# Kernel optimization log

Hardware: AMD Instinct MI355X
Metric: run time of the kernel (lower is better)

The kernel has to match this reference:

```python
import jax, jax.numpy as jnp
import numpy as np

B, T, H, V = 64, 48, 512, 32000


def _uni(k, shape, fan_in):
    s = 1.0 / np.sqrt(fan_in)
    return jax.random.uniform(k, shape, jnp.float32, -s, s)


def setup_inputs() -> dict:
    key = jax.random.key(0)
    ks = jax.random.split(key, 21)
    inp = {
        "feat": jax.random.normal(ks[0], (B, T, H), jnp.float32),
        "caption": jax.random.normal(ks[1], (B, T, H), jnp.float32),
        "ids": jax.random.randint(ks[2], (B, T), 0, V),
    }
    i = 3
    for name, in_dim in (("1", H), ("2", 2 * H), ("d1", H), ("d2", 2 * H)):
        inp["w_ih" + name] = _uni(ks[i], (4 * H, in_dim), H); i += 1
        inp["w_hh" + name] = _uni(ks[i], (4 * H, H), H); i += 1
        inp["b_ih" + name] = _uni(ks[i], (4 * H,), H); i += 1
        inp["b_hh" + name] = _uni(ks[i], (4 * H,), H); i += 1
    inp["w_o"] = _uni(ks[i], (V, H), H); i += 1
    inp["b_o"] = _uni(ks[i], (V,), H)
    return inp


def lstm_cell(x, h, c, w_ih, w_hh, b_ih, b_hh):
    # PyTorch LSTMCell: gates in i, f, g, o order
    g = x @ w_ih.T + b_ih + h @ w_hh.T + b_hh
    gi, gf, gg, go = jnp.split(g, 4, axis=-1)
    c_new = jax.nn.sigmoid(gf) * c + jax.nn.sigmoid(gi) * jnp.tanh(gg)
    h_new = jax.nn.sigmoid(go) * jnp.tanh(c_new)
    return h_new, c_new


def reference(feat, caption, ids,
              w_ih1, w_hh1, b_ih1, b_hh1,
              w_ih2, w_hh2, b_ih2, b_hh2,
              w_ihd1, w_hhd1, b_ihd1, b_hhd1,
              w_ihd2, w_hhd2, b_ihd2, b_hhd2,
              w_o, b_o):
    pad = jnp.zeros((B, H), feat.dtype)
    z = jnp.zeros((B, H), feat.dtype)

    def enc_step(carry, x):
        h1, c1, h2, c2 = carry
        h1, c1 = lstm_cell(x, h1, c1, w_ih1, w_hh1, b_ih1, b_hh1)
        h2, c2 = lstm_cell(jnp.concatenate([pad, h1], 1), h2, c2,
                           w_ih2, w_hh2, b_ih2, b_hh2)
        return (h1, c1, h2, c2), None

    carry, _ = jax.lax.scan(enc_step, (z, z, z, z), jnp.swapaxes(feat, 0, 1))

    def dec_step(carry, xs):
        h1, c1, h2, c2 = carry
        cap, tgt = xs
        h1, c1 = lstm_cell(pad, h1, c1, w_ihd1, w_hhd1, b_ihd1, b_hhd1)
        h2, c2 = lstm_cell(jnp.concatenate([cap, h1], 1), h2, c2,
                           w_ihd2, w_hhd2, b_ihd2, b_hhd2)
        logits = h2 @ w_o.T + b_o  # [B, V]
        lp = jax.nn.log_softmax(logits, axis=-1)
        ce = -jnp.take_along_axis(lp, tgt[:, None], axis=1)[:, 0].mean()
        return (h1, c1, h2, c2), ce

    caps = jnp.swapaxes(caption[:, : T - 1, :], 0, 1)  # [T-1, B, H]
    tgts = jnp.swapaxes(ids[:, 1:T], 0, 1)             # [T-1, B]
    _, ces = jax.lax.scan(dec_step, carry, (caps, tgts))
    # total_loss += sum(mean_ce) / batch_size (word_loss is already a mean)
    return jnp.sum(ces) / B
```

## Files before the change

kernel.cpp:

```cpp
#include <hip/hip_runtime.h>
#include <math.h>

#define B_ 64
#define T_ 48
#define H_ 512
#define V_ 32000
#define G_ 2048
#define BH_ (B_*H_)
#define BG_ (B_*G_)

typedef short short8 __attribute__((ext_vector_type(8)));
typedef float f32x4 __attribute__((ext_vector_type(4)));

__device__ __forceinline__ float sigmoidf_(float x){ return 1.f/(1.f+__expf(-x)); }

__device__ __forceinline__ unsigned short f2bf(float f){
  unsigned u = __float_as_uint(f);
  u += 0x7fffu + ((u>>16)&1u);
  return (unsigned short)(u>>16);
}
__device__ __forceinline__ float bf2f(unsigned short u){
  return __uint_as_float(((unsigned)u)<<16);
}

__device__ __forceinline__ short8 cvt8(const float* g){
  float4 a = *(const float4*)g;
  float4 b = *(const float4*)(g+4);
  short8 v;
  v[0]=(short)f2bf(a.x); v[1]=(short)f2bf(a.y); v[2]=(short)f2bf(a.z); v[3]=(short)f2bf(a.w);
  v[4]=(short)f2bf(b.x); v[5]=(short)f2bf(b.y); v[6]=(short)f2bf(b.z); v[7]=(short)f2bf(b.w);
  return v;
}

__global__ void init_kernel(unsigned short* h1_0, unsigned short* h2_0, unsigned* flags){
  int i = blockIdx.x*256 + threadIdx.x;
  short8 z = {0,0,0,0,0,0,0,0};
  if (i < 4096) ((short8*)h1_0)[i] = z;
  else          ((short8*)h2_0)[i-4096] = z;
  if (i < 1152) flags[i] = 0u;
}

__global__ void cvt_cat_kernel(const float* __restrict__ s0, int ld0, int off0,
                               const float* __restrict__ s1, int ld1, int off1,
                               unsigned short* __restrict__ dst, int dld, long total8)
{
  int cols8 = dld >> 3;
  for (long i = blockIdx.x*256 + threadIdx.x; i < total8; i += (long)gridDim.x*256){
    int r = (int)(i / cols8);
    int k = (int)(i - (long)r*cols8) * 8;
    short8 v = (k < 512 || !s1) ? cvt8(s0 + (long)r*ld0 + off0 + k)
                                : cvt8(s1 + (long)r*ld1 + off1 + (k-512));
    *(short8*)(dst + (long)r*dld + k) = v;
  }
}

__global__ void bias_sum_kernel(const float* a1, const float* a2, float* o1,
                                const float* b1, const float* b2, float* o2){
  int n = blockIdx.x*256 + threadIdx.x;
  if (n < G_){ o1[n] = a1[n] + a2[n]; o2[n] = b1[n] + b2[n]; }
}

__global__ __launch_bounds__(512,1) void mm_pre_kernel(
    const float* __restrict__ A, int a_bstride,
    const unsigned short* __restrict__ Wbf,
    const float* __restrict__ bA, const float* __restrict__ bB,
    unsigned short* __restrict__ out)
{
  const int s = blockIdx.x, n0 = blockIdx.y*256;
  const int t = threadIdx.x, w = t>>6, l = t&63, ln = l&15, lk = l>>4;
  __shared__ short8 smA[64*64];
  __shared__ short8 smB[256*8];

  const float* af32 = A + (long)s*H_;

  f32x4 acc[4][2];
#pragma unroll
  for (int mf=0; mf<4; ++mf)
#pragma unroll
    for (int nf=0; nf<2; ++nf) acc[mf][nf] = (f32x4){0.f,0.f,0.f,0.f};

#pragma unroll
  for (int i=0;i<8;++i){ int e=i*4096+t*8; int m=e>>9, k=e&511;
    smA[m*64 + ((k>>3)^(m&7))] = cvt8(&af32[(long)m*a_bstride + k]); }

  for (int kc=0; kc<8; ++kc){
    __syncthreads();
#pragma unroll
    for (int i=0;i<4;++i){ int e=i*4096+t*8; int n=e>>6, k=e&63;
      smB[n*8 + ((k>>3)^(n&7))] = *(const short8*)(Wbf + (long)(n0+n)*512 + kc*64 + k); }
    __syncthreads();
#pragma unroll
    for (int ks2=0; ks2<2; ++ks2){
#pragma unroll
      for (int nf=0; nf<2; ++nf){
        int n = w*32 + nf*16 + ln;
        short8 bfr = smB[n*8 + ((ks2*4+lk)^(n&7))];
#pragma unroll
        for (int mf=0; mf<4; ++mf){
          int m = mf*16+ln;
          short8 afr = smA[m*64 + (((kc*2+ks2)*4+lk)^(m&7))];
          acc[mf][nf] = __builtin_amdgcn_mfma_f32_16x16x32_bf16(afr, bfr, acc[mf][nf], 0,0,0);
        }
      }
    }
  }
#pragma unroll
  for (int nf=0; nf<2; ++nf){
    int n = n0 + w*32 + nf*16 + ln;
    float bias = bA[n] + bB[n];
#pragma unroll
    for (int mf=0; mf<4; ++mf)
#pragma unroll
      for (int r=0; r<4; ++r){
        int m = mf*16 + lk*4 + r;
        out[(long)s*BG_ + (long)m*G_ + n] = f2bf(acc[mf][nf][r] + bias);
      }
  }
}

__global__ __launch_bounds__(256,1) void fused_chain_kernel(
    const unsigned short* __restrict__ w1e, const unsigned short* __restrict__ w1d,
    const unsigned short* __restrict__ w2e, const unsigned short* __restrict__ w2d,
    const unsigned short* __restrict__ x1b,
    const unsigned short* __restrict__ capqb,
    const float* __restrict__ bd1s, const float* __restrict__ b2es,
    unsigned short* __restrict__ h1, unsigned short* __restrict__ h2,
    unsigned* __restrict__ flags)
{
  const int bc = blockIdx.x;
  const int isL2 = (bc >= 32);
  const int cb = bc & 31;
  const int t = threadIdx.x;
  const int wv = t>>6, l = t&63, ln = l&15, lk = l>>4;

  __shared__ short8 smA[64*128];
  __shared__ float gbuf[4][16][68];
  __shared__ float c_lds[16][68];
  unsigned short* stash = (unsigned short*)&smA[0];

  short8 W[32];
  const int col = wv*512 + cb*16 + ln;
  if (isL2){
    const long wrow = (long)col * 1024;
#pragma unroll
    for (int ks=0; ks<32; ++ks) W[ks] = *(const short8*)(w2e + wrow + ks*32 + lk*8);
  } else {
    const long wrow = (long)col * 512;
#pragma unroll
    for (int ks=0; ks<16; ++ks){
      W[ks]    = *(const short8*)(w1e + wrow + ks*32 + lk*8);
      W[16+ks] = *(const short8*)(w1d + wrow + ks*32 + lk*8);
    }
  }
  const float bext = isL2 ? b2es[col] : bd1s[col];

  for (int i=t; i<16*68; i+=256) (&c_lds[0][0])[i] = 0.f;

  for (int s=0; s<96; ++s){
    if (isL2 && s == 49){
      const long wrow = (long)col * 1024;
#pragma unroll
      for (int ks=0; ks<32; ++ks) W[ks] = *(const short8*)(w2d + wrow + ks*32 + lk*8);
    }
    const int active = isL2 ? (s>=1) : (s<95);
    if (active){
      if (!isL2){
        const unsigned short* hp = h1 + (long)s*BH_;
#pragma unroll
        for (int i=0;i<16;++i){ int e=i*2048+t*8; int m=e>>9, k=e&511;
          smA[m*128 + ((k>>3)^(m&7))] = *(const short8*)(hp + m*512 + k); }
      } else {
        const unsigned short* hpA = h2 + (long)(s-1)*BH_;
        const unsigned short* hpB = h1 + (long)s*BH_;
#pragma unroll
        for (int i=0;i<16;++i){ int e=i*2048+t*8; int m=e>>9, k=e&511;
          smA[m*128 + ((k>>3)^(m&7))]      = *(const short8*)(hpA + m*512 + k);
          smA[m*128 + ((k>>3)^(m&7)) + 64] = *(const short8*)(hpB + m*512 + k);
        }
      }

      const int dec = isL2 ? ((s-1)>=48) : (s>=48);
      float prev[4][4];
      if (!isL2){
        if (s < 48){
          const unsigned short* pp = x1b + (long)s*BG_ + col;
#pragma unroll
          for (int mf=0;mf<4;++mf)
#pragma unroll
            for (int r=0;r<4;++r) prev[mf][r] = bf2f(pp[(long)(mf*16+lk*4+r)*G_]);
        } else {
#pragma unroll
          for (int mf=0;mf<4;++mf)
#pragma unroll
            for (int r=0;r<4;++r) prev[mf][r] = bext;
        }
      } else {
        int s2 = s-1;
        if (s2 < 48){
#pragma unroll
          for (int mf=0;mf<4;++mf)
#pragma unroll
            for (int r=0;r<4;++r) prev[mf][r] = bext;
        } else {
          const unsigned short* pp = capqb + (long)(s2-48)*BG_ + col;
#pragma unroll
          for (int mf=0;mf<4;++mf)
#pragma unroll
            for (int r=0;r<4;++r) prev[mf][r] = bf2f(pp[(long)(mf*16+lk*4+r)*G_]);
        }
      }
      __syncthreads();

      f32x4 acc[4];
#pragma unroll
      for (int mf=0;mf<4;++mf) acc[mf] = (f32x4){0.f,0.f,0.f,0.f};

      if (isL2){
#pragma unroll
        for (int ks=0; ks<32; ++ks)
#pragma unroll
          for (int mf=0; mf<4; ++mf){
            int m = mf*16+ln;
            acc[mf] = __builtin_amdgcn_mfma_f32_16x16x32_bf16(
              smA[m*128 + ((ks*4+lk)^(m&7))], W[ks], acc[mf], 0,0,0);
          }
      } else if (!dec){
#pragma unroll
        for (int ks=0; ks<16; ++ks)
#pragma unroll
          for (int mf=0; mf<4; ++mf){
            int m = mf*16+ln;
            acc[mf] = __builtin_amdgcn_mfma_f32_16x16x32_bf16(
              smA[m*128 + ((ks*4+lk)^(m&7))], W[ks], acc[mf], 0,0,0);
          }
      } else {
#pragma unroll
        for (int ks=0; ks<16; ++ks)
#pragma unroll
          for (int mf=0; mf<4; ++mf){
            int m = mf*16+ln;
            acc[mf] = __builtin_amdgcn_mfma_f32_16x16x32_bf16(
              smA[m*128 + ((ks*4+lk)^(m&7))], W[16+ks], acc[mf], 0,0,0);
          }
      }

#pragma unroll
      for (int mf=0;mf<4;++mf)
#pragma unroll
        for (int r=0;r<4;++r) acc[mf][r] += prev[mf][r];

#pragma unroll
      for (int mf=0;mf<4;++mf) *(f32x4*)&gbuf[wv][ln][mf*16+lk*4] = acc[mf];
      __syncthreads();

      {
        int n = t&15, m0 = (t>>4)*4;
        float4 gi = *(float4*)&gbuf[0][n][m0];
        float4 gf = *(float4*)&gbuf[1][n][m0];
        float4 gg = *(float4*)&gbuf[2][n][m0];
        float4 go = *(float4*)&gbuf[3][n][m0];
        float4 c4 = *(float4*)&c_lds[n][m0];
        float cn[4];
        float a_i[4]={gi.x,gi.y,gi.z,gi.w}, a_f[4]={gf.x,gf.y,gf.z,gf.w};
        float a_g[4]={gg.x,gg.y,gg.z,gg.w}, a_o[4]={go.x,go.y,go.z,go.w};
        float ci[4]={c4.x,c4.y,c4.z,c4.w};
#pragma unroll
        for (int j=0;j<4;++j){
          float i_ = sigmoidf_(a_i[j]), f_ = sigmoidf_(a_f[j]), o_ = sigmoidf_(a_o[j]);
          float g_ = tanhf(a_g[j]);
          cn[j] = f_*ci[j] + i_*g_;
          stash[(m0+j)*24 + n] = f2bf(o_*tanhf(cn[j]));
        }
        *(float4*)&c_lds[n][m0] = make_float4(cn[0],cn[1],cn[2],cn[3]);
      }
      __syncthreads();
      {
        unsigned short* ho = (isL2 ? (h2 + (long)s*BH_) : (h1 + (long)(s+1)*BH_)) + cb*16;
        int m = t>>2, q = t&3;
        unsigned long long v = *(const unsigned long long*)&stash[m*24 + q*4];
        __hip_atomic_store((unsigned long long*)(ho + (long)m*512 + q*4), v,
                           __ATOMIC_RELAXED, __HIP_MEMORY_SCOPE_AGENT);
      }
    }

    if (s < 95){
      unsigned g = (unsigned)(s+1);
      __syncthreads();
      if (t == 0)
        __hip_atomic_store(&flags[bc*16], g, __ATOMIC_RELAXED, __HIP_MEMORY_SCOPE_AGENT);
      if (t < 64){
        while (__hip_atomic_load(&flags[t*16], __ATOMIC_RELAXED, __HIP_MEMORY_SCOPE_AGENT) < g)
          __builtin_amdgcn_s_sleep(1);
      }
      __syncthreads();
    }
  }
}

__global__ __launch_bounds__(512,1) void ce_vt_kernel(
    const unsigned short* __restrict__ h2_bf, const unsigned short* __restrict__ wo_bf,
    const float* __restrict__ b_o, const int* __restrict__ ids,
    float* __restrict__ partial, float* __restrict__ tgt)
{
  const int vt = blockIdx.x, v0 = vt*128;
  const int t = threadIdx.x, wv = t>>6, l = t&63, ln = l&15, lk = l>>4;
  __shared__ short8 smB[128*64];
  __shared__ short8 smAc[64*8];
  __shared__ float red[8][64];
  __shared__ int tid_s[64];

  for (int i = t; i < 128*64; i += 512){
    int n = i >> 6, c = i & 63;
    smB[n*64 + ((c & 56) | ((c & 7) ^ (n & 7)))] =
        *(const short8*)(wo_bf + (long)(v0+n)*512 + c*8);
  }
  const int nn = wv*16 + ln;
  const float bo = b_o[v0 + nn];
  __syncthreads();

  for (int td = 0; td < 47; ++td){
    if (t < 64) tid_s[t] = ids[t*T_ + td + 1];
    const unsigned short* hp = h2_bf + (long)(49+td)*BH_;

    f32x4 acc[4];
#pragma unroll
    for (int mf=0;mf<4;++mf) acc[mf] = (f32x4){0.f,0.f,0.f,0.f};

    for (int kc=0; kc<8; ++kc){
      __syncthreads();
      { int m = t>>3, c = t&7;
        smAc[m*8 + (c ^ (m&7))] = *(const short8*)(hp + m*512 + kc*64 + c*8); }
      __syncthreads();
#pragma unroll
      for (int ks2=0; ks2<2; ++ks2){
        short8 bfr = smB[nn*64 + kc*8 + ((ks2*4+lk)^(nn&7))];
#pragma unroll
        for (int mf=0; mf<4; ++mf){
          int m = mf*16+ln;
          short8 afr = smAc[m*8 + ((ks2*4+lk)^(m&7))];
          acc[mf] = __builtin_amdgcn_mfma_f32_16x16x32_bf16(afr, bfr, acc[mf], 0,0,0);
        }
      }
    }

    float se[4][4];
#pragma unroll
    for (int mf=0; mf<4; ++mf)
#pragma unroll
      for (int r=0;r<4;++r){
        int m = mf*16 + lk*4 + r;
        float lg = acc[mf][r] + bo;
        se[mf][r] = __expf(lg);
        if (v0 + nn == tid_s[m]) tgt[td*64 + m] = lg;
      }
#pragma unroll
    for (int off=1; off<16; off<<=1)
#pragma unroll
      for (int mf=0; mf<4; ++mf)
#pragma unroll
        for (int r=0;r<4;++r) se[mf][r] += __shfl_xor(se[mf][r], off);
    if (ln == 0){
#pragma unroll
      for (int mf=0; mf<4; ++mf)
        *(f32x4*)&red[wv][mf*16 + lk*4] = (f32x4){se[mf][0],se[mf][1],se[mf][2],se[mf][3]};
    }
    __syncthreads();
    if (t < 64){
      float ssum = 0.f;
#pragma unroll
      for (int w2=0; w2<8; ++w2) ssum += red[w2][t];
      partial[(long)vt*3008 + td*64 + t] = ssum;
    }
  }
}

__global__ void ce_combine(const float* __restrict__ partial, const float* __restrict__ tgt,
                           float* __restrict__ ce_row){
  int r = blockIdx.x*256 + threadIdx.x;
  if (r < 3008){
    float s = 0.f;
    for (int i=0;i<250;++i) s += partial[(long)i*3008 + r];
    ce_row[r] = __logf(s) - tgt[r];
  }
}

__global__ void ce_final(const float* __restrict__ ce_row, float* __restrict__ out){
  __shared__ float red[256];
  float s = 0.f;
  for (int i=threadIdx.x; i<3008; i+=256) s += ce_row[i];
  red[threadIdx.x] = s;
  __syncthreads();
  for (int off=128; off>0; off>>=1){
    if (threadIdx.x < off) red[threadIdx.x] += red[threadIdx.x + off];
    __syncthreads();
  }
  if (threadIdx.x == 0) out[0] = red[0] * (1.0f/4096.0f);
}

extern "C" void kernel_launch(void* const* d_in, const int* in_sizes, int n_in,
                              void* d_out, int out_size, void* d_ws, size_t ws_size,
                              hipStream_t stream)
{
  (void)in_sizes; (void)n_in; (void)out_size; (void)ws_size;
  const float* feat    = (const float*)d_in[0];
  const float* caption = (const float*)d_in[1];
  const int*   ids     = (const int*)d_in[2];
  const float* w_ih1  = (const float*)d_in[3];
  const float* w_hh1  = (const float*)d_in[4];
  const float* b_ih1  = (const float*)d_in[5];
  const float* b_hh1  = (const float*)d_in[6];
  const float* w_ih2  = (const float*)d_in[7];
  const float* w_hh2  = (const float*)d_in[8];
  const float* b_ih2  = (const float*)d_in[9];
  const float* b_hh2  = (const float*)d_in[10];
  const float* w_hhd1 = (const float*)d_in[12];
  const float* b_ihd1 = (const float*)d_in[13];
  const float* b_hhd1 = (const float*)d_in[14];
  const float* w_ihd2 = (const float*)d_in[15];
  const float* w_hhd2 = (const float*)d_in[16];
  const float* b_ihd2 = (const float*)d_in[17];
  const float* b_hhd2 = (const float*)d_in[18];
  const float* w_o    = (const float*)d_in[19];
  const float* b_o    = (const float*)d_in[20];

  char* p = (char*)d_ws;
  unsigned short* h1    = (unsigned short*)p; p += 96L*BH_*2;
  unsigned short* h2    = (unsigned short*)p; p += 96L*BH_*2;
  unsigned short* w2e   = (unsigned short*)p; p += 2048L*1024*2;
  unsigned short* w2d   = (unsigned short*)p; p += 2048L*1024*2;
  char* alias0 = p;
  unsigned short* w1e   = (unsigned short*)p; p += 2048L*512*2;
  unsigned short* w1d   = (unsigned short*)p; p += 2048L*512*2;
  unsigned short* wx1   = (unsigned short*)p; p += 2048L*512*2;
  unsigned short* wcap  = (unsigned short*)p; p += 2048L*512*2;
  unsigned short* x1b   = (unsigned short*)p; p += 48L*BG_*2;
  unsigned short* capqb = (unsigned short*)p; p += 47L*BG_*2;
  unsigned short* wo_bf = (unsigned short*)alias0;
  float* bd1s  = (float*)p; p += 2048*4;
  float* b2es  = (float*)p; p += 2048*4;
  float* partial = (float*)p; p += 250L*3008*4;
  float* tgt   = (float*)p; p += 3008*4;
  float* ce_row= (float*)p; p += 3008*4;
  unsigned* flags = (unsigned*)p; p += 1152*4;

  init_kernel<<<32, 256, 0, stream>>>(h1, h2, flags);

  cvt_cat_kernel<<<256, 256, 0, stream>>>(w_hh1, 512, 0, nullptr, 0, 0, w1e, 512, 2048L*64);
  cvt_cat_kernel<<<256, 256, 0, stream>>>(w_hhd1, 512, 0, nullptr, 0, 0, w1d, 512, 2048L*64);
  cvt_cat_kernel<<<256, 256, 0, stream>>>(w_hh2, 512, 0, w_ih2, 1024, 512, w2e, 1024, 2048L*128);
  cvt_cat_kernel<<<256, 256, 0, stream>>>(w_hhd2, 512, 0, w_ihd2, 1024, 512, w2d, 1024, 2048L*128);
  cvt_cat_kernel<<<256, 256, 0, stream>>>(w_ih1, 512, 0, nullptr, 0, 0, wx1, 512, 2048L*64);
  cvt_cat_kernel<<<256, 256, 0, stream>>>(w_ihd2, 1024, 0, nullptr, 0, 0, wcap, 512, 2048L*64);
  bias_sum_kernel<<<8, 256, 0, stream>>>(b_ihd1, b_hhd1, bd1s, b_ih2, b_hh2, b2es);

  mm_pre_kernel<<<dim3(48,8), 512, 0, stream>>>(feat, T_*H_, wx1, b_ih1, b_hh1, x1b);
  mm_pre_kernel<<<dim3(47,8), 512, 0, stream>>>(caption, T_*H_, wcap, b_ihd2, b_hhd2, capqb);

  fused_chain_kernel<<<64, 256, 0, stream>>>(w1e, w1d, w2e, w2d, x1b, capqb, bd1s, b2es, h1, h2, flags);

  cvt_cat_kernel<<<512, 256, 0, stream>>>(w_o, 512, 0, nullptr, 0, 0, wo_bf, 512, 32000L*64);

  ce_vt_kernel<<<250, 512, 0, stream>>>(h2, wo_bf, b_o, ids, partial, tgt);
  ce_combine<<<12, 256, 0, stream>>>(partial, tgt, ce_row);
  ce_final<<<1, 256, 0, stream>>>(ce_row, (float*)d_out);
}
```

Before: 1.580 ms.

## Overlap decoder CE projection with LSTM chain in persistent mega-kernel

Merges the many weight-conversion, bias and init launches into one prep kernel and combines the two input-projection GEMMs into a single launch. The main change folds the vocabulary-projection cross-entropy into the recurrent chain kernel. 186 extra CE blocks each hold a 128-column slice of w_o in LDS and spin on per-step flags, so they consume each decoder h2 as soon as it is produced instead of waiting for the whole chain. wo_bf no longer aliases the chain weights, which costs extra workspace. The design relies on all 250 blocks being co-resident, or the spinning CE blocks could starve the chain.

```diff
diff --git a/kernel.cpp b/kernel.cpp
--- a/kernel.cpp
+++ b/kernel.cpp
@@ -8,6 +8,7 @@
 #define G_ 2048
 #define BH_ (B_*H_)
 #define BG_ (B_*G_)
+#define NCE_ 186
 
 typedef short short8 __attribute__((ext_vector_type(8)));
 typedef float f32x4 __attribute__((ext_vector_type(4)));
@@ -32,46 +33,71 @@
   return v;
 }
 
-__global__ void init_kernel(unsigned short* h1_0, unsigned short* h2_0, unsigned* flags){
-  int i = blockIdx.x*256 + threadIdx.x;
-  short8 z = {0,0,0,0,0,0,0,0};
-  if (i < 4096) ((short8*)h1_0)[i] = z;
-  else          ((short8*)h2_0)[i-4096] = z;
-  if (i < 1152) flags[i] = 0u;
-}
-
-__global__ void cvt_cat_kernel(const float* __restrict__ s0, int ld0, int off0,
-                               const float* __restrict__ s1, int ld1, int off1,
-                               unsigned short* __restrict__ dst, int dld, long total8)
+#define CEGO_(i) ((64+(i))*16)
+
+__global__ void prep_kernel(
+    const float* __restrict__ w_hh1, const float* __restrict__ w_hhd1,
+    const float* __restrict__ w_hh2, const float* __restrict__ w_ih2,
+    const float* __restrict__ w_hhd2, const float* __restrict__ w_ihd2,
+    const float* __restrict__ w_ih1, const float* __restrict__ w_o,
+    const float* __restrict__ b_ihd1, const float* __restrict__ b_hhd1,
+    const float* __restrict__ b_ih2,  const float* __restrict__ b_hh2,
+    unsigned short* w1e, unsigned short* w1d, unsigned short* w2e, unsigned short* w2d,
+    unsigned short* wx1, unsigned short* wcap, unsigned short* wo_bf,
+    float* bd1s, float* b2es,
+    unsigned short* h1_0, unsigned short* h2_0, unsigned* flags)
 {
-  int cols8 = dld >> 3;
-  for (long i = blockIdx.x*256 + threadIdx.x; i < total8; i += (long)gridDim.x*256){
-    int r = (int)(i / cols8);
-    int k = (int)(i - (long)r*cols8) * 8;
-    short8 v = (k < 512 || !s1) ? cvt8(s0 + (long)r*ld0 + off0 + k)
-                                : cvt8(s1 + (long)r*ld1 + off1 + (k-512));
-    *(short8*)(dst + (long)r*dld + k) = v;
+  const int b = blockIdx.x, t = threadIdx.x;
+  if (b < 64){
+    for (long i = b*256+t; i < 2048L*64; i += 64L*256){ int r=(int)(i>>6), k=(int)(i&63)*8;
+      *(short8*)(w1e + (long)r*512 + k) = cvt8(w_hh1 + (long)r*512 + k); }
+  } else if (b < 128){
+    for (long i = (b-64)*256+t; i < 2048L*64; i += 64L*256){ int r=(int)(i>>6), k=(int)(i&63)*8;
+      *(short8*)(w1d + (long)r*512 + k) = cvt8(w_hhd1 + (long)r*512 + k); }
+  } else if (b < 256){
+    for (long i = (b-128)*256+t; i < 2048L*128; i += 128L*256){ int r=(int)(i>>7), k=(int)(i&127)*8;
+      short8 v = (k<512)? cvt8(w_hh2+(long)r*512+k) : cvt8(w_ih2+(long)r*1024+512+(k-512));
+      *(short8*)(w2e + (long)r*1024 + k) = v; }
+  } else if (b < 384){
+    for (long i = (b-256)*256+t; i < 2048L*128; i += 128L*256){ int r=(int)(i>>7), k=(int)(i&127)*8;
+      short8 v = (k<512)? cvt8(w_hhd2+(long)r*512+k) : cvt8(w_ihd2+(long)r*1024+512+(k-512));
+      *(short8*)(w2d + (long)r*1024 + k) = v; }
+  } else if (b < 448){
+    for (long i = (b-384)*256+t; i < 2048L*64; i += 64L*256){ int r=(int)(i>>6), k=(int)(i&63)*8;
+      *(short8*)(wx1 + (long)r*512 + k) = cvt8(w_ih1 + (long)r*512 + k); }
+  } else if (b < 512){
+    for (long i = (b-448)*256+t; i < 2048L*64; i += 64L*256){ int r=(int)(i>>6), k=(int)(i&63)*8;
+      *(short8*)(wcap + (long)r*512 + k) = cvt8(w_ihd2 + (long)r*1024 + k); }
+  } else if (b < 1012){
+    for (long i = (long)(b-512)*256+t; i < 32000L*64; i += 500L*256){ int r=(int)(i>>6), k=(int)(i&63)*8;
+      *(short8*)(wo_bf + (long)r*512 + k) = cvt8(w_o + (long)r*512 + k); }
+  } else if (b < 1020){
+    int n = (b-1012)*256 + t;
+    bd1s[n] = b_ihd1[n] + b_hhd1[n];
+    b2es[n] = b_ih2[n] + b_hh2[n];
+  } else {
+    short8 z = {0,0,0,0,0,0,0,0};
+    for (int i=(b-1020)*256+t; i<4096; i+=4*256){ ((short8*)h1_0)[i]=z; ((short8*)h2_0)[i]=z; }
+    for (int i=(b-1020)*256+t; i<4096; i+=4*256) flags[i] = 0u;
   }
 }
 
-__global__ void bias_sum_kernel(const float* a1, const float* a2, float* o1,
-                                const float* b1, const float* b2, float* o2){
-  int n = blockIdx.x*256 + threadIdx.x;
-  if (n < G_){ o1[n] = a1[n] + a2[n]; o2[n] = b1[n] + b2[n]; }
-}
-
-__global__ __launch_bounds__(512,1) void mm_pre_kernel(
-    const float* __restrict__ A, int a_bstride,
-    const unsigned short* __restrict__ Wbf,
-    const float* __restrict__ bA, const float* __restrict__ bB,
-    unsigned short* __restrict__ out)
+__global__ __launch_bounds__(512,1) void mm_pre2_kernel(
+    const float* __restrict__ feat, const float* __restrict__ caption,
+    const unsigned short* __restrict__ wx1, const unsigned short* __restrict__ wcap,
+    const float* __restrict__ b_ih1, const float* __restrict__ b_hh1,
+    const float* __restrict__ b_ihd2, const float* __restrict__ b_hhd2,
+    unsigned short* __restrict__ x1b, unsigned short* __restrict__ capqb)
 {
   const int s = blockIdx.x, n0 = blockIdx.y*256;
   const int t = threadIdx.x, w = t>>6, l = t&63, ln = l&15, lk = l>>4;
   __shared__ short8 smA[64*64];
   __shared__ short8 smB[256*8];
 
-  const float* af32 = A + (long)s*H_;
+  const float* af32; const unsigned short* Wbf; const float* bA; const float* bB;
+  unsigned short* out;
+  if (s < 48){ af32 = feat + (long)s*H_;          Wbf = wx1;  bA = b_ih1;  bB = b_hh1;  out = x1b  + (long)s*BG_; }
+  else       { af32 = caption + (long)(s-48)*H_;  Wbf = wcap; bA = b_ihd2; bB = b_hhd2; out = capqb + (long)(s-48)*BG_; }
 
   f32x4 acc[4][2];
 #pragma unroll
@@ -81,7 +107,7 @@
 
 #pragma unroll
   for (int i=0;i<8;++i){ int e=i*4096+t*8; int m=e>>9, k=e&511;
-    smA[m*64 + ((k>>3)^(m&7))] = cvt8(&af32[(long)m*a_bstride + k]); }
+    smA[m*64 + ((k>>3)^(m&7))] = cvt8(&af32[(long)m*(T_*H_) + k]); }
 
   for (int kc=0; kc<8; ++kc){
     __syncthreads();
@@ -113,263 +139,295 @@
 #pragma unroll
       for (int r=0; r<4; ++r){
         int m = mf*16 + lk*4 + r;
-        out[(long)s*BG_ + (long)m*G_ + n] = f2bf(acc[mf][nf][r] + bias);
+        out[(long)m*G_ + n] = f2bf(acc[mf][nf][r] + bias);
       }
   }
 }
 
-__global__ __launch_bounds__(256,1) void fused_chain_kernel(
+__global__ __launch_bounds__(256,1) void mega_kernel(
     const unsigned short* __restrict__ w1e, const unsigned short* __restrict__ w1d,
     const unsigned short* __restrict__ w2e, const unsigned short* __restrict__ w2d,
-    const unsigned short* __restrict__ x1b,
-    const unsigned short* __restrict__ capqb,
+    const unsigned short* __restrict__ x1b, const unsigned short* __restrict__ capqb,
     const float* __restrict__ bd1s, const float* __restrict__ b2es,
     unsigned short* __restrict__ h1, unsigned short* __restrict__ h2,
+    const unsigned short* __restrict__ wo_bf, const float* __restrict__ b_o,
+    const int* __restrict__ ids,
+    float* __restrict__ partial, float* __restrict__ tgt,
     unsigned* __restrict__ flags)
 {
-  const int bc = blockIdx.x;
-  const int isL2 = (bc >= 32);
-  const int cb = bc & 31;
-  const int t = threadIdx.x;
-  const int wv = t>>6, l = t&63, ln = l&15, lk = l>>4;
-
   __shared__ short8 smA[64*128];
   __shared__ float gbuf[4][16][68];
   __shared__ float c_lds[16][68];
-  unsigned short* stash = (unsigned short*)&smA[0];
-
-  short8 W[32];
-  const int col = wv*512 + cb*16 + ln;
-  if (isL2){
-    const long wrow = (long)col * 1024;
-#pragma unroll
-    for (int ks=0; ks<32; ++ks) W[ks] = *(const short8*)(w2e + wrow + ks*32 + lk*8);
-  } else {
-    const long wrow = (long)col * 512;
-#pragma unroll
-    for (int ks=0; ks<16; ++ks){
-      W[ks]    = *(const short8*)(w1e + wrow + ks*32 + lk*8);
-      W[16+ks] = *(const short8*)(w1d + wrow + ks*32 + lk*8);
+  const int bcg = blockIdx.x;
+  const int t = threadIdx.x;
+  const int wv = t>>6, l = t&63, ln = l&15, lk = l>>4;
+
+  if (bcg < 64){
+    const int bc = bcg;
+    const int isL2 = (bc >= 32);
+    const int cb = bc & 31;
+    unsigned short* stash = (unsigned short*)&smA[0];
+
+    short8 W[32];
+    const int col = wv*512 + cb*16 + ln;
+    if (isL2){
+      const long wrow = (long)col * 1024;
+#pragma unroll
+      for (int ks=0; ks<32; ++ks) W[ks] = *(const short8*)(w2e + wrow + ks*32 + lk*8);
+    } else {
+      const long wrow = (long)col * 512;
+#pragma unroll
+      for (int ks=0; ks<16; ++ks){
+        W[ks]    = *(const short8*)(w1e + wrow + ks*32 + lk*8);
+        W[16+ks] = *(const short8*)(w1d + wrow + ks*32 + lk*8);
+      }
     }
-  }
-  const float bext = isL2 ? b2es[col] : bd1s[col];
-
-  for (int i=t; i<16*68; i+=256) (&c_lds[0][0])[i] = 0.f;
-
-  for (int s=0; s<96; ++s){
-    if (isL2 && s == 49){
-      const long wrow = (long)col * 1024;
-#pragma unroll
-      for (int ks=0; ks<32; ++ks) W[ks] = *(const short8*)(w2d + wrow + ks*32 + lk*8);
-    }
-    const int active = isL2 ? (s>=1) : (s<95);
-    if (active){
-      if (!isL2){
-        const unsigned short* hp = h1 + (long)s*BH_;
-#pragma unroll
-        for (int i=0;i<16;++i){ int e=i*2048+t*8; int m=e>>9, k=e&511;
-          smA[m*128 + ((k>>3)^(m&7))] = *(const short8*)(hp + m*512 + k); }
-      } else {
-        const unsigned short* hpA = h2 + (long)(s-1)*BH_;
-        const unsigned short* hpB = h1 + (long)s*BH_;
-#pragma unroll
-        for (int i=0;i<16;++i){ int e=i*2048+t*8; int m=e>>9, k=e&511;
-          smA[m*128 + ((k>>3)^(m&7))]      = *(const short8*)(hpA + m*512 + k);
-          smA[m*128 + ((k>>3)^(m&7)) + 64] = *(const short8*)(hpB + m*512 + k);
-        }
-      }
-
-      const int dec = isL2 ? ((s-1)>=48) : (s>=48);
-      float prev[4][4];
-      if (!isL2){
-        if (s < 48){
-          const unsigned short* pp = x1b + (long)s*BG_ + col;
-#pragma unroll
-          for (int mf=0;mf<4;++mf)
-#pragma unroll
-            for (int r=0;r<4;++r) prev[mf][r] = bf2f(pp[(long)(mf*16+lk*4+r)*G_]);
+    const float bext = isL2 ? b2es[col] : bd1s[col];
+
+    for (int i=t; i<16*68; i+=256) (&c_lds[0][0])[i] = 0.f;
+
+    for (int s=0; s<96; ++s){
+      if (isL2 && s == 49){
+        const long wrow = (long)col * 1024;
+#pragma unroll
+        for (int ks=0; ks<32; ++ks) W[ks] = *(const short8*)(w2d + wrow + ks*32 + lk*8);
+      }
+      const int active = isL2 ? (s>=1) : (s<95);
+      if (active){
+        if (!isL2){
+          const unsigned short* hp = h1 + (long)s*BH_;
+#pragma unroll
+          for (int i=0;i<16;++i){ int e=i*2048+t*8; int m=e>>9, k=e&511;
+            smA[m*128 + ((k>>3)^(m&7))] = *(const short8*)(hp + m*512 + k); }
         } else {
-#pragma unroll
-          for (int mf=0;mf<4;++mf)
-#pragma unroll
-            for (int r=0;r<4;++r) prev[mf][r] = bext;
-        }
-      } else {
-        int s2 = s-1;
-        if (s2 < 48){
-#pragma unroll
-          for (int mf=0;mf<4;++mf)
-#pragma unroll
-            for (int r=0;r<4;++r) prev[mf][r] = bext;
+          const unsigned short* hpA = h2 + (long)(s-1)*BH_;
+          const unsigned short* hpB = h1 + (long)s*BH_;
+#pragma unroll
+          for (int i=0;i<16;++i){ int e=i*2048+t*8; int m=e>>9, k=e&511;
+            smA[m*128 + ((k>>3)^(m&7))]      = *(const short8*)(hpA + m*512 + k);
+            smA[m*128 + ((k>>3)^(m&7)) + 64] = *(const short8*)(hpB + m*512 + k);
+          }
+        }
+
+        const int dec = isL2 ? ((s-1)>=48) : (s>=48);
+        float prev[4][4];
+        if (!isL2){
+          if (s < 48){
+            const unsigned short* pp = x1b + (long)s*BG_ + col;
+#pragma unroll
+            for (int mf=0;mf<4;++mf)
+#pragma unroll
+              for (int r=0;r<4;++r) prev[mf][r] = bf2f(pp[(long)(mf*16+lk*4+r)*G_]);
+          } else {
+#pragma unroll
+            for (int mf=0;mf<4;++mf)
+#pragma unroll
+              for (int r=0;r<4;++r) prev[mf][r] = bext;
+          }
         } else {
-          const unsigned short* pp = capqb + (long)(s2-48)*BG_ + col;
-#pragma unroll
-          for (int mf=0;mf<4;++mf)
-#pragma unroll
-            for (int r=0;r<4;++r) prev[mf][r] = bf2f(pp[(long)(mf*16+lk*4+r)*G_]);
-        }
-      }
-      __syncthreads();
-
-      f32x4 acc[4];
-#pragma unroll
-      for (int mf=0;mf<4;++mf) acc[mf] = (f32x4){0.f,0.f,0.f,0.f};
-
-      if (isL2){
-#pragma unroll
-        for (int ks=0; ks<32; ++ks)
-#pragma unroll
-          for (int mf=0; mf<4; ++mf){
-            int m = mf*16+ln;
-            acc[mf] = __builtin_amdgcn_mfma_f32_16x16x32_bf16(
-              smA[m*128 + ((ks*4+lk)^(m&7))], W[ks], acc[mf], 0,0,0);
+          int s2 = s-1;
+          if (s2 < 48){
+#pragma unroll
+            for (int mf=0;mf<4;++mf)
+#pragma unroll
+              for (int r=0;r<4;++r) prev[mf][r] = bext;
+          } else {
+            const unsigned short* pp = capqb + (long)(s2-48)*BG_ + col;
+#pragma unroll
+            for (int mf=0;mf<4;++mf)
+#pragma unroll
+              for (int r=0;r<4;++r) prev[mf][r] = bf2f(pp[(long)(mf*16+lk*4+r)*G_]);
           }
-      } else if (!dec){
-#pragma unroll
-        for (int ks=0; ks<16; ++ks)
-#pragma unroll
-          for (int mf=0; mf<4; ++mf){
-            int m = mf*16+ln;
-            acc[mf] = __builtin_amdgcn_mfma_f32_16x16x32_bf16(
-              smA[m*128 + ((ks*4+lk)^(m&7))], W[ks], acc[mf], 0,0,0);
+        }
+        __syncthreads();
+
+        f32x4 acc[4];
+#pragma unroll
+        for (int mf=0;mf<4;++mf) acc[mf] = (f32x4){0.f,0.f,0.f,0.f};
+
+        if (isL2){
+#pragma unroll
+          for (int ks=0; ks<32; ++ks)
+#pragma unroll
+            for (int mf=0; mf<4; ++mf){
+              int m = mf*16+ln;
+              acc[mf] = __builtin_amdgcn_mfma_f32_16x16x32_bf16(
+                smA[m*128 + ((ks*4+lk)^(m&7))], W[ks], acc[mf], 0,0,0);
+            }
+        } else if (!dec){
+#pragma unroll
+          for (int ks=0; ks<16; ++ks)
+#pragma unroll
+            for (int mf=0; mf<4; ++mf){
+              int m = mf*16+ln;
+              acc[mf] = __builtin_amdgcn_mfma_f32_16x16x32_bf16(
+                smA[m*128 + ((ks*4+lk)^(m&7))], W[ks], acc[mf], 0,0,0);
+            }
+        } else {
+#pragma unroll
+          for (int ks=0; ks<16; ++ks)
+#pragma unroll
+            for (int mf=0; mf<4; ++mf){
+              int m = mf*16+ln;
+              acc[mf] = __builtin_amdgcn_mfma_f32_16x16x32_bf16(
+                smA[m*128 + ((ks*4+lk)^(m&7))], W[16+ks], acc[mf], 0,0,0);
+            }
+        }
+
+#pragma unroll
+        for (int mf=0;mf<4;++mf)
+#pragma unroll
+          for (int r=0;r<4;++r) acc[mf][r] += prev[mf][r];
+
+#pragma unroll
+        for (int mf=0;mf<4;++mf) *(f32x4*)&gbuf[wv][ln][mf*16+lk*4] = acc[mf];
+        __syncthreads();
+
+        {
+          int n = t&15, m0 = (t>>4)*4;
+          float4 gi = *(float4*)&gbuf[0][n][m0];
+          float4 gf = *(float4*)&gbuf[1][n][m0];
+          float4 gg = *(float4*)&gbuf[2][n][m0];
+          float4 go = *(float4*)&gbuf[3][n][m0];
+          float4 c4 = *(float4*)&c_lds[n][m0];
+          float cn[4];
+          float a_i[4]={gi.x,gi.y,gi.z,gi.w}, a_f[4]={gf.x,gf.y,gf.z,gf.w};
+          float a_g[4]={gg.x,gg.y,gg.z,gg.w}, a_o[4]={go.x,go.y,go.z,go.w};
+          float ci[4]={c4.x,c4.y,c4.z,c4.w};
+#pragma unroll
+          for (int j=0;j<4;++j){
+            float i_ = sigmoidf_(a_i[j]), f_ = sigmoidf_(a_f[j]), o_ = sigmoidf_(a_o[j]);
+            float g_ = tanhf(a_g[j]);
+            cn[j] = f_*ci[j] + i_*g_;
+            stash[(m0+j)*24 + n] = f2bf(o_*tanhf(cn[j]));
           }
-      } else {
-#pragma unroll
-        for (int ks=0; ks<16; ++ks)
-#pragma unroll
-          for (int mf=0; mf<4; ++mf){
-            int m = mf*16+ln;
-            acc[mf] = __builtin_amdgcn_mfma_f32_16x16x32_bf16(
-              smA[m*128 + ((ks*4+lk)^(m&7))], W[16+ks], acc[mf], 0,0,0);
-          }
-      }
-
-#pragma unroll
-      for (int mf=0;mf<4;++mf)
-#pragma unroll
-        for (int r=0;r<4;++r) acc[mf][r] += prev[mf][r];
-
-#pragma unroll
-      for (int mf=0;mf<4;++mf) *(f32x4*)&gbuf[wv][ln][mf*16+lk*4] = acc[mf];
-      __syncthreads();
-
-      {
-        int n = t&15, m0 = (t>>4)*4;
-        float4 gi = *(float4*)&gbuf[0][n][m0];
-        float4 gf = *(float4*)&gbuf[1][n][m0];
-        float4 gg = *(float4*)&gbuf[2][n][m0];
-        float4 go = *(float4*)&gbuf[3][n][m0];
-        float4 c4 = *(float4*)&c_lds[n][m0];
-        float cn[4];
-        float a_i[4]={gi.x,gi.y,gi.z,gi.w}, a_f[4]={gf.x,gf.y,gf.z,gf.w};
-        float a_g[4]={gg.x,gg.y,gg.z,gg.w}, a_o[4]={go.x,go.y,go.z,go.w};
-        float ci[4]={c4.x,c4.y,c4.z,c4.w};
-#pragma unroll
-        for (int j=0;j<4;++j){
-          float i_ = sigmoidf_(a_i[j]), f_ = sigmoidf_(a_f[j]), o_ = sigmoidf_(a_o[j]);
-          float g_ = tanhf(a_g[j]);
-          cn[j] = f_*ci[j] + i_*g_;
-          stash[(m0+j)*24 + n] = f2bf(o_*tanhf(cn[j]));
-        }
-        *(float4*)&c_lds[n][m0] = make_float4(cn[0],cn[1],cn[2],cn[3]);
-      }
-      __syncthreads();
-      {
-        unsigned short* ho = (isL2 ? (h2 + (long)s*BH_) : (h1 + (long)(s+1)*BH_)) + cb*16;
-        int m = t>>2, q = t&3;
-        unsigned long long v = *(const unsigned long long*)&stash[m*24 + q*4];
-        __hip_atomic_store((unsigned long long*)(ho + (long)m*512 + q*4), v,
-                           __ATOMIC_RELAXED, __HIP_MEMORY_SCOPE_AGENT);
-      }
-    }
-
-    if (s < 95){
-      unsigned g = (unsigned)(s+1);
-      __syncthreads();
-      if (t == 0)
-        __hip_atomic_store(&flags[bc*16], g, __ATOMIC_RELAXED, __HIP_MEMORY_SCOPE_AGENT);
-      if (t < 64){
-        while (__hip_atomic_load(&flags[t*16], __ATOMIC_RELAXED, __HIP_MEMORY_SCOPE_AGENT) < g)
-          __builtin_amdgcn_s_sleep(1);
-      }
-      __syncthreads();
-    }
-  }
-}
-
-__global__ __launch_bounds__(512,1) void ce_vt_kernel(
-    const unsigned short* __restrict__ h2_bf, const unsigned short* __restrict__ wo_bf,
-    const float* __restrict__ b_o, const int* __restrict__ ids,
-    float* __restrict__ partial, float* __restrict__ tgt)
-{
-  const int vt = blockIdx.x, v0 = vt*128;
-  const int t = threadIdx.x, wv = t>>6, l = t&63, ln = l&15, lk = l>>4;
-  __shared__ short8 smB[128*64];
-  __shared__ short8 smAc[64*8];
-  __shared__ float red[8][64];
-  __shared__ int tid_s[64];
-
-  for (int i = t; i < 128*64; i += 512){
-    int n = i >> 6, c = i & 63;
-    smB[n*64 + ((c & 56) | ((c & 7) ^ (n & 7)))] =
-        *(const short8*)(wo_bf + (long)(v0+n)*512 + c*8);
-  }
-  const int nn = wv*16 + ln;
-  const float bo = b_o[v0 + nn];
-  __syncthreads();
-
-  for (int td = 0; td < 47; ++td){
-    if (t < 64) tid_s[t] = ids[t*T_ + td + 1];
-    const unsigned short* hp = h2_bf + (long)(49+td)*BH_;
-
-    f32x4 acc[4];
-#pragma unroll
-    for (int mf=0;mf<4;++mf) acc[mf] = (f32x4){0.f,0.f,0.f,0.f};
-
-    for (int kc=0; kc<8; ++kc){
-      __syncthreads();
-      { int m = t>>3, c = t&7;
-        smAc[m*8 + (c ^ (m&7))] = *(const short8*)(hp + m*512 + kc*64 + c*8); }
-      __syncthreads();
-#pragma unroll
-      for (int ks2=0; ks2<2; ++ks2){
-        short8 bfr = smB[nn*64 + kc*8 + ((ks2*4+lk)^(nn&7))];
-#pragma unroll
-        for (int mf=0; mf<4; ++mf){
-          int m = mf*16+ln;
-          short8 afr = smAc[m*8 + ((ks2*4+lk)^(m&7))];
-          acc[mf] = __builtin_amdgcn_mfma_f32_16x16x32_bf16(afr, bfr, acc[mf], 0,0,0);
-        }
-      }
-    }
-
-    float se[4][4];
-#pragma unroll
-    for (int mf=0; mf<4; ++mf)
-#pragma unroll
-      for (int r=0;r<4;++r){
-        int m = mf*16 + lk*4 + r;
-        float lg = acc[mf][r] + bo;
-        se[mf][r] = __expf(lg);
-        if (v0 + nn == tid_s[m]) tgt[td*64 + m] = lg;
-      }
-#pragma unroll
-    for (int off=1; off<16; off<<=1)
-#pragma unroll
-      for (int mf=0; mf<4; ++mf)
-#pragma unroll
-        for (int r=0;r<4;++r) se[mf][r] += __shfl_xor(se[mf][r], off);
-    if (ln == 0){
-#pragma unroll
-      for (int mf=0; mf<4; ++mf)
-        *(f32x4*)&red[wv][mf*16 + lk*4] = (f32x4){se[mf][0],se[mf][1],se[mf][2],se[mf][3]};
+          *(float4*)&c_lds[n][m0] = make_float4(cn[0],cn[1],cn[2],cn[3]);
+        }
+        __syncthreads();
+        {
+          unsigned short* ho = (isL2 ? (h2 + (long)s*BH_) : (h1 + (long)(s+1)*BH_)) + cb*16;
+          int m = t>>2, q = t&3;
+          unsigned long long v = *(const unsigned long long*)&stash[m*24 + q*4];
+          __hip_atomic_store((unsigned long long*)(ho + (long)m*512 + q*4), v,
+                             __ATOMIC_RELAXED, __HIP_MEMORY_SCOPE_AGENT);
+        }
+      }
+
+      if (s < 95){
+        unsigned g = (unsigned)(s+1);
+        __syncthreads();
+        if (t == 0)
+          __hip_atomic_store(&flags[bcg*16], g, __ATOMIC_RELAXED, __HIP_MEMORY_SCOPE_AGENT);
+        if (t < 64){
+          while (__hip_atomic_load(&flags[t*16], __ATOMIC_RELAXED, __HIP_MEMORY_SCOPE_AGENT) < g)
+            __builtin_amdgcn_s_sleep(1);
+        }
+        __syncthreads();
+        if (bcg == 32 && g >= 50 && t < NCE_)
+          __hip_atomic_store(&flags[CEGO_(t)], g, __ATOMIC_RELAXED, __HIP_MEMORY_SCOPE_AGENT);
+      }
     }
     __syncthreads();
-    if (t < 64){
-      float ssum = 0.f;
-#pragma unroll
-      for (int w2=0; w2<8; ++w2) ssum += red[w2][t];
-      partial[(long)vt*3008 + td*64 + t] = ssum;
+    if (t == 0)
+      __hip_atomic_store(&flags[bcg*16], 96u, __ATOMIC_RELAXED, __HIP_MEMORY_SCOPE_AGENT);
+    if (bcg == 32){
+      if (t >= 32 && t < 64){
+        while (__hip_atomic_load(&flags[t*16], __ATOMIC_RELAXED, __HIP_MEMORY_SCOPE_AGENT) < 96u)
+          __builtin_amdgcn_s_sleep(1);
+      }
+      __syncthreads();
+      if (t < NCE_)
+        __hip_atomic_store(&flags[CEGO_(t)], 96u, __ATOMIC_RELAXED, __HIP_MEMORY_SCOPE_AGENT);
+    }
+  } else {
+    const int ceid = bcg - 64;
+    short8* smB  = smA;
+    short8* smAc = (short8*)&gbuf[0][0][0];
+    float*  redf = &c_lds[0][0];
+    int*    tid_s = (int*)(&c_lds[0][0]) + 256;
+
+    for (int slice = ceid; slice < 250; slice += NCE_){
+      const int vt = slice, v0 = vt*128;
+      __syncthreads();
+      for (int i = t; i < 128*64; i += 256){
+        int n = i >> 6, c = i & 63;
+        smB[n*64 + ((c & 56) | ((c & 7) ^ (n & 7)))] =
+            *(const short8*)(wo_bf + (long)(v0+n)*512 + c*8);
+      }
+
+      for (int td = 0; td < 47; ++td){
+        if (t == 0){
+          unsigned need = (unsigned)(50 + td);
+          while (__hip_atomic_load(&flags[CEGO_(ceid)], __ATOMIC_RELAXED, __HIP_MEMORY_SCOPE_AGENT) < need)
+            __builtin_amdgcn_s_sleep(8);
+        }
+        if (t < 64) tid_s[t] = ids[t*T_ + td + 1];
+        const unsigned short* hp = h2 + (long)(49+td)*BH_;
+
+        f32x4 acc[4][2];
+#pragma unroll
+        for (int mf=0; mf<4; ++mf)
+#pragma unroll
+          for (int nf=0; nf<2; ++nf) acc[mf][nf] = (f32x4){0.f,0.f,0.f,0.f};
+
+        for (int kc=0; kc<8; ++kc){
+          __syncthreads();
+#pragma unroll
+          for (int i=0;i<2;++i){ int e=i*256+t; int m=e>>3, c=e&7;
+            smAc[m*8 + (c ^ (m&7))] = *(const short8*)(hp + m*512 + kc*64 + c*8); }
+          __syncthreads();
+#pragma unroll
+          for (int ks2=0; ks2<2; ++ks2){
+#pragma unroll
+            for (int nf=0; nf<2; ++nf){
+              int n = wv*32 + nf*16 + ln;
+              short8 bfr = smB[n*64 + kc*8 + ((ks2*4+lk)^(n&7))];
+#pragma unroll
+              for (int mf=0; mf<4; ++mf){
+                int m = mf*16+ln;
+                short8 afr = smAc[m*8 + ((ks2*4+lk)^(m&7))];
+                acc[mf][nf] = __builtin_amdgcn_mfma_f32_16x16x32_bf16(afr, bfr, acc[mf][nf], 0,0,0);
+              }
+            }
+          }
+        }
+
+        float se[4][4];
+#pragma unroll
+        for (int mf=0; mf<4; ++mf)
+#pragma unroll
+          for (int r=0;r<4;++r) se[mf][r] = 0.f;
+#pragma unroll
+        for (int nf=0; nf<2; ++nf){
+          int ng = v0 + wv*32 + nf*16 + ln;
+          float bo = b_o[ng];
+#pragma unroll
+          for (int mf=0; mf<4; ++mf)
+#pragma unroll
+            for (int r=0;r<4;++r){
+              int m = mf*16 + lk*4 + r;
+              float lg = acc[mf][nf][r] + bo;
+              se[mf][r] += __expf(lg);
+              if (ng == tid_s[m]) tgt[td*64 + m] = lg;
+            }
+        }
+#pragma unroll
+        for (int off=1; off<16; off<<=1)
+#pragma unroll
+          for (int mf=0; mf<4; ++mf)
+#pragma unroll
+            for (int r=0;r<4;++r) se[mf][r] += __shfl_xor(se[mf][r], off);
+        if (ln == 0){
+#pragma unroll
+          for (int mf=0; mf<4; ++mf)
+            *(f32x4*)&redf[wv*64 + mf*16 + lk*4] = (f32x4){se[mf][0],se[mf][1],se[mf][2],se[mf][3]};
+        }
+        __syncthreads();
+        if (t < 64){
+          float ssum = redf[t] + redf[64+t] + redf[128+t] + redf[192+t];
+          partial[(long)vt*3008 + td*64 + t] = ssum;
+        }
+      }
     }
   }
 }
@@ -426,41 +484,34 @@
   char* p = (char*)d_ws;
   unsigned short* h1    = (unsigned short*)p; p += 96L*BH_*2;
   unsigned short* h2    = (unsigned short*)p; p += 96L*BH_*2;
+  unsigned short* w1e   = (unsigned short*)p; p += 2048L*512*2;
+  unsigned short* w1d   = (unsigned short*)p; p += 2048L*512*2;
   unsigned short* w2e   = (unsigned short*)p; p += 2048L*1024*2;
   unsigned short* w2d   = (unsigned short*)p; p += 2048L*1024*2;
-  char* alias0 = p;
-  unsigned short* w1e   = (unsigned short*)p; p += 2048L*512*2;
-  unsigned short* w1d   = (unsigned short*)p; p += 2048L*512*2;
   unsigned short* wx1   = (unsigned short*)p; p += 2048L*512*2;
   unsigned short* wcap  = (unsigned short*)p; p += 2048L*512*2;
   unsigned short* x1b   = (unsigned short*)p; p += 48L*BG_*2;
   unsigned short* capqb = (unsigned short*)p; p += 47L*BG_*2;
-  unsigned short* wo_bf = (unsigned short*)alias0;
+  unsigned short* wo_bf = (unsigned short*)p; p += 32000L*512*2;
   float* bd1s  = (float*)p; p += 2048*4;
   float* b2es  = (float*)p; p += 2048*4;
   float* partial = (float*)p; p += 250L*3008*4;
   float* tgt   = (float*)p; p += 3008*4;
   float* ce_row= (float*)p; p += 3008*4;
-  unsigned* flags = (unsigned*)p; p += 1152*4;
-
-  init_kernel<<<32, 256, 0, stream>>>(h1, h2, flags);
-
-  cvt_cat_kernel<<<256, 256, 0, stream>>>(w_hh1, 512, 0, nullptr, 0, 0, w1e, 512, 2048L*64);
-  cvt_cat_kernel<<<256, 256, 0, stream>>>(w_hhd1, 512, 0, nullptr, 0, 0, w1d, 512, 2048L*64);
-  cvt_cat_kernel<<<256, 256, 0, stream>>>(w_hh2, 512, 0, w_ih2, 1024, 512, w2e, 1024, 2048L*128);
-  cvt_cat_kernel<<<256, 256, 0, stream>>>(w_hhd2, 512, 0, w_ihd2, 1024, 512, w2d, 1024, 2048L*128);
-  cvt_cat_kernel<<<256, 256, 0, stream>>>(w_ih1, 512, 0, nullptr, 0, 0, wx1, 512, 2048L*64);
-  cvt_cat_kernel<<<256, 256, 0, stream>>>(w_ihd2, 1024, 0, nullptr, 0, 0, wcap, 512, 2048L*64);
-  bias_sum_kernel<<<8, 256, 0, stream>>>(b_ihd1, b_hhd1, bd1s, b_ih2, b_hh2, b2es);
-
-  mm_pre_kernel<<<dim3(48,8), 512, 0, stream>>>(feat, T_*H_, wx1, b_ih1, b_hh1, x1b);
-  mm_pre_kernel<<<dim3(47,8), 512, 0, stream>>>(caption, T_*H_, wcap, b_ihd2, b_hhd2, capqb);
-
-  fused_chain_kernel<<<64, 256, 0, stream>>>(w1e, w1d, w2e, w2d, x1b, capqb, bd1s, b2es, h1, h2, flags);
-
-  cvt_cat_kernel<<<512, 256, 0, stream>>>(w_o, 512, 0, nullptr, 0, 0, wo_bf, 512, 32000L*64);
-
-  ce_vt_kernel<<<250, 512, 0, stream>>>(h2, wo_bf, b_o, ids, partial, tgt);
+  unsigned* flags = (unsigned*)p; p += 4096*4;
+
+  prep_kernel<<<1024, 256, 0, stream>>>(
+      w_hh1, w_hhd1, w_hh2, w_ih2, w_hhd2, w_ihd2, w_ih1, w_o,
+      b_ihd1, b_hhd1, b_ih2, b_hh2,
+      w1e, w1d, w2e, w2d, wx1, wcap, wo_bf, bd1s, b2es, h1, h2, flags);
+
+  mm_pre2_kernel<<<dim3(95,8), 512, 0, stream>>>(
+      feat, caption, wx1, wcap, b_ih1, b_hh1, b_ihd2, b_hhd2, x1b, capqb);
+
+  mega_kernel<<<64+NCE_, 256, 0, stream>>>(
+      w1e, w1d, w2e, w2d, x1b, capqb, bd1s, b2es, h1, h2,
+      wo_bf, b_o, ids, partial, tgt, flags);
+
   ce_combine<<<12, 256, 0, stream>>>(partial, tgt, ce_row);
   ce_final<<<1, 256, 0, stream>>>(ce_row, (float*)d_out);
 }
```

Result: faster. 1.537 ms (-2.7%).
